# Kernel optimization log

Hardware: AMD Instinct MI355X
Metric: run time of the kernel (lower is better)

Reference implementation:

```python
import jax, jax.numpy as jnp
import numpy as np

DIM = 1024
QK = 128
HID = 2048  # int(2 * dim)
B, N = 4, 2048
EPS = 1e-5

def setup_inputs() -> dict:
    key = jax.random.key(0)
    ks = jax.random.split(key, 8)
    std = 0.02
    return {
        "x": jax.random.normal(ks[0], (B, N, DIM), jnp.float32),
        "ln_scale": jnp.ones((DIM,), jnp.float32),
        "ln_bias": jnp.zeros((DIM,), jnp.float32),
        "W_hidden": jax.random.normal(ks[1], (DIM, 2 * HID), jnp.float32) * std,
        "b_hidden": jnp.zeros((2 * HID,), jnp.float32),
        "W_qk": jax.random.normal(ks[2], (DIM, QK), jnp.float32) * std,
        "b_qk": jnp.zeros((QK,), jnp.float32),
        "os_weight": jax.random.normal(ks[3], (2, QK), jnp.float32) * std,
        "os_bias": jnp.zeros((2, QK), jnp.float32),
        "W_out": jax.random.normal(ks[4], (HID, DIM), jnp.float32) * std,
        "b_out": jnp.zeros((DIM,), jnp.float32),
    }

def reference(x, ln_scale, ln_bias, W_hidden, b_hidden, W_qk, b_qk,
              os_weight, os_bias, W_out, b_out):
    n = x.shape[1]
    # LayerNorm over last dim
    mu = jnp.mean(x, axis=-1, keepdims=True)
    var = jnp.mean(jnp.square(x - mu), axis=-1, keepdims=True)
    xn = (x - mu) / jnp.sqrt(var + EPS) * ln_scale + ln_bias
    # to_hidden: Linear + SiLU, chunk into v, gate
    hid = jax.nn.silu(xn @ W_hidden + b_hidden)          # [B,N,2*HID]
    v, gate = hid[..., :HID], hid[..., HID:]
    # to_qk: Linear + SiLU
    qk = jax.nn.silu(xn @ W_qk + b_qk)                   # [B,N,QK]
    # offset_scale: per-head elementwise affine -> q, k
    qk2 = qk[..., None, :] * os_weight + os_bias         # [B,N,2,QK]
    q, k = qk2[..., 0, :], qk2[..., 1, :]
    # ReLU^2 attention
    sim = jnp.einsum('bid,bjd->bij', q, k) / n           # [B,N,N]
    attn = jnp.square(jax.nn.relu(sim))
    out = jnp.einsum('bij,bjd->bid', attn, v)            # [B,N,HID]
    out = out * gate
    return out @ W_out + b_out
```

## Files before the change

### kernel.cpp

```cpp
#include <hip/hip_runtime.h>
#include <math.h>

#define DIMX 1024
#define QKD  128
#define HIDD 2048
#define BATCH 4
#define SEQ  2048

typedef __bf16 bf16;
typedef __bf16 bf16x8 __attribute__((ext_vector_type(8)));
typedef __bf16 bf16x4v __attribute__((ext_vector_type(4)));
typedef float f32x4 __attribute__((ext_vector_type(4)));

__device__ __forceinline__ float siluf(float v) { return v / (1.f + expf(-v)); }
__device__ __forceinline__ void splitf(float x, bf16& h, bf16& l) {
    h = (bf16)x;
    l = (bf16)(x - (float)h);
}
__device__ __forceinline__ f32x4 mfma16(bf16x8 a, bf16x8 b, f32x4 c) {
    return __builtin_amdgcn_mfma_f32_16x16x32_bf16(a, b, c, 0, 0, 0);
}

typedef __attribute__((address_space(1))) const void cg_void;
typedef __attribute__((address_space(3))) void lds_void_t;
__device__ __forceinline__ void gload16(const bf16* g, bf16* l) {
    __builtin_amdgcn_global_load_lds((cg_void*)g, (lds_void_t*)l, 16, 0, 0);
}

template<int N> __device__ __forceinline__ void wait_vm() {
    if constexpr (N == 0)  asm volatile("s_waitcnt vmcnt(0)" ::: "memory");
    if constexpr (N == 3)  asm volatile("s_waitcnt vmcnt(3)" ::: "memory");
    if constexpr (N == 4)  asm volatile("s_waitcnt vmcnt(4)" ::: "memory");
    if constexpr (N == 6)  asm volatile("s_waitcnt vmcnt(6)" ::: "memory");
    if constexpr (N == 8)  asm volatile("s_waitcnt vmcnt(8)" ::: "memory");
}

#define SB0 __builtin_amdgcn_sched_barrier(0)

__global__ __launch_bounds__(256) void ln_split(const float* __restrict__ x,
                                                const float* __restrict__ scale,
                                                const float* __restrict__ bias,
                                                bf16* __restrict__ xh,
                                                bf16* __restrict__ xl) {
    const int row = blockIdx.x;
    const float4 v = reinterpret_cast<const float4*>(x + (size_t)row * DIMX)[threadIdx.x];
    float s  = v.x + v.y + v.z + v.w;
    float ss = v.x * v.x + v.y * v.y + v.z * v.z + v.w * v.w;
    #pragma unroll
    for (int off = 32; off; off >>= 1) {
        s  += __shfl_down(s, off);
        ss += __shfl_down(ss, off);
    }
    __shared__ float ls[4], lss[4];
    const int wid = threadIdx.x >> 6, lane = threadIdx.x & 63;
    if (lane == 0) { ls[wid] = s; lss[wid] = ss; }
    __syncthreads();
    if (threadIdx.x == 0) {
        float a = ls[0] + ls[1] + ls[2] + ls[3];
        float b = lss[0] + lss[1] + lss[2] + lss[3];
        float mu  = a / DIMX;
        float var = b / DIMX - mu * mu;
        ls[0]  = mu;
        lss[0] = rsqrtf(var + 1e-5f);
    }
    __syncthreads();
    const float mu = ls[0], rs = lss[0];
    const float4 sc = reinterpret_cast<const float4*>(scale)[threadIdx.x];
    const float4 bi = reinterpret_cast<const float4*>(bias)[threadIdx.x];
    float o[4];
    o[0] = (v.x - mu) * rs * sc.x + bi.x;
    o[1] = (v.y - mu) * rs * sc.y + bi.y;
    o[2] = (v.z - mu) * rs * sc.z + bi.z;
    o[3] = (v.w - mu) * rs * sc.w + bi.w;
    bf16x4v h, l;
    #pragma unroll
    for (int i = 0; i < 4; ++i) { bf16 hh, ll; splitf(o[i], hh, ll); h[i] = hh; l[i] = ll; }
    *reinterpret_cast<bf16x4v*>(xh + (size_t)row * DIMX + threadIdx.x * 4) = h;
    *reinterpret_cast<bf16x4v*>(xl + (size_t)row * DIMX + threadIdx.x * 4) = l;
}

__global__ __launch_bounds__(256) void wsplitT(const float* __restrict__ W, int K, int N,
                                               bf16* __restrict__ Th, bf16* __restrict__ Tl) {
    __shared__ float tile[32][33];
    const int bx = blockIdx.x * 32;
    const int by = blockIdx.y * 32;
    const int tx = threadIdx.x & 31, ty = threadIdx.x >> 5;
    #pragma unroll
    for (int r = 0; r < 32; r += 8)
        tile[ty + r][tx] = W[(size_t)(by + ty + r) * N + bx + tx];
    __syncthreads();
    #pragma unroll
    for (int r = 0; r < 32; r += 8) {
        const float v = tile[tx][ty + r];
        bf16 h, l; splitf(v, h, l);
        Th[(size_t)(bx + ty + r) * K + by + tx] = h;
        if (Tl) Tl[(size_t)(bx + ty + r) * K + by + tx] = l;
    }
}

template<int EPI, int BN>
__global__ __launch_bounds__(512) void gmm2(
    const bf16* __restrict__ A, int lda, long long sA,
    const bf16* __restrict__ B, int ldb, long long sB,
    bf16* __restrict__ O, int ldo, long long sO,
    bf16* __restrict__ G, int ldg, long long sG,
    float* __restrict__ F, int ldf,
    const float* __restrict__ e0,
    int K) {

    constexpr int BM = 256, BK = 32;
    constexpr int AE = BM * BK;
    constexpr int BE = BN * BK;
    constexpr int CHA = AE / (512 * 8);
    constexpr int CHB = BE / (512 * 8);
    constexpr int L = CHA + CHB;
    constexpr int WN = BN / 4;
    constexpr int MI = 8, NI = WN / 16;

    __shared__ __align__(16) bf16 lds[4 * (AE + BE)];

    const int z = blockIdx.z;
    A += (size_t)sA * z;
    B += (size_t)sB * z;
    bf16* Oz = O ? O + (size_t)sO * z : nullptr;
    bf16* Gz = G ? G + (size_t)sG * z : nullptr;

    const int tid = threadIdx.x;
    const int l = tid & 63, w = tid >> 6;
    const int wr = w >> 2, wc = w & 3;
    const int lr = l & 15, ls4 = l >> 4;
    const int bm = blockIdx.y * BM, bn = blockIdx.x * BN;

    const bf16* aptr[CHA];
    #pragma unroll
    for (int c = 0; c < CHA; ++c) {
        const int flat = c * 512 + tid;
        const int row = flat >> 2;
        const int slot = (flat & 3) ^ ((row >> 1) & 3);
        aptr[c] = A + (size_t)(bm + row) * lda + slot * 8;
    }
    const bf16* bptr[CHB];
    #pragma unroll
    for (int c = 0; c < CHB; ++c) {
        const int flat = c * 512 + tid;
        const int row = flat >> 2;
        const int slot = (flat & 3) ^ ((row >> 1) & 3);
        bptr[c] = B + (size_t)(bn + row) * ldb + slot * 8;
    }

    int aoff[MI], boff[NI];
    #pragma unroll
    for (int i = 0; i < MI; ++i) {
        const int row = wr * 128 + i * 16 + lr;
        aoff[i] = row * BK + (ls4 ^ ((row >> 1) & 3)) * 8;
    }
    #pragma unroll
    for (int j = 0; j < NI; ++j) {
        const int row = wc * WN + j * 16 + lr;
        boff[j] = row * BK + (ls4 ^ ((row >> 1) & 3)) * 8;
    }

    const int NT = K / BK;
    f32x4 acc[MI][NI] = {};

    auto stage = [&](int tile) {
        const int buf = tile & 3;
        bf16* ab = lds + buf * (AE + BE);
        bf16* bb = ab + AE;
        #pragma unroll
        for (int c = 0; c < CHA; ++c)
            gload16(aptr[c] + tile * BK, ab + (c * 512 + w * 64) * 8);
        #pragma unroll
        for (int c = 0; c < CHB; ++c)
            gload16(bptr[c] + tile * BK, bb + (c * 512 + w * 64) * 8);
    };

    stage(0); SB0;
    stage(1); SB0;
    stage(2); SB0;

    for (int t = 0; t < NT; ++t) {
        const int ahead = NT - 1 - t;
        if (ahead >= 2)      wait_vm<2 * L>();
        else if (ahead == 1) wait_vm<L>();
        else                 wait_vm<0>();
        __builtin_amdgcn_s_barrier();
        SB0;

        const int buf = t & 3;
        const bf16* ab = lds + buf * (AE + BE);
        const bf16* bb = ab + AE;
        bf16x8 bfr[NI], afr[MI];
        #pragma unroll
        for (int j = 0; j < NI; ++j)
            bfr[j] = *reinterpret_cast<const bf16x8*>(&bb[boff[j]]);
        #pragma unroll
        for (int i = 0; i < MI; ++i)
            afr[i] = *reinterpret_cast<const bf16x8*>(&ab[aoff[i]]);
        asm volatile("s_waitcnt lgkmcnt(0)" ::: "memory");
        SB0;
        if (t + 3 < NT) { stage(t + 3); }
        SB0;
        __builtin_amdgcn_s_setprio(1);
        #pragma unroll
        for (int i = 0; i < MI; ++i)
            #pragma unroll
            for (int j = 0; j < NI; ++j)
                acc[i][j] = mfma16(afr[i], bfr[j], acc[i][j]);
        __builtin_amdgcn_s_setprio(0);
        SB0;
    }

    #pragma unroll
    for (int i = 0; i < MI; ++i) {
        const int mf = bm + wr * 128 + i * 16 + ls4 * 4;
        #pragma unroll
        for (int j = 0; j < NI; ++j) {
            const int nn = bn + wc * WN + j * 16 + lr;
            const f32x4 a = acc[i][j];
            if constexpr (EPI == 0) {
                float s[4];
                #pragma unroll
                for (int r = 0; r < 4; ++r) s[r] = siluf(a[r] + e0[nn]);
                bf16x4v h;
                #pragma unroll
                for (int r = 0; r < 4; ++r) h[r] = (bf16)s[r];
                if (nn < HIDD)
                    *reinterpret_cast<bf16x4v*>(&Oz[(size_t)nn * ldo + mf]) = h;
                else
                    *reinterpret_cast<bf16x4v*>(&Gz[(size_t)(nn - HIDD) * ldg + mf]) = h;
            } else if constexpr (EPI == 3) {
                const bf16x4v g4 = *reinterpret_cast<const bf16x4v*>(&Gz[(size_t)nn * ldg + mf]);
                #pragma unroll
                for (int r = 0; r < 4; ++r)
                    Oz[(size_t)(mf + r) * ldo + nn] = (bf16)(a[r] * (float)g4[r]);
            } else {
                #pragma unroll
                for (int r = 0; r < 4; ++r)
                    F[(size_t)(mf + r) * ldf + nn] = a[r] + e0[nn];
            }
        }
    }
}

template<int EPI, bool SPLIT, int MI, int NI>
__global__ __launch_bounds__(256) void gmm(
    const bf16* __restrict__ Ah, const bf16* __restrict__ Al, int lda, long long sA,
    const bf16* __restrict__ Bh, const bf16* __restrict__ Bl, int ldb, long long sB,
    bf16* __restrict__ O, int ldo, long long sO,
    bf16* __restrict__ O2, bf16* __restrict__ O3, bf16* __restrict__ O4,
    const float* __restrict__ e0, const float* __restrict__ e1, const float* __restrict__ e2,
    int K, float scale) {

    constexpr int TM = MI * 32, TN = NI * 32;
    constexpr int CHA = TM / 64, CHB = TN / 64;
    __shared__ __align__(16) bf16 As[TM * 32];
    __shared__ __align__(16) bf16 Bs[TN * 32];

    const int z = blockIdx.z;
    Ah += (size_t)sA * z;
    if (SPLIT) Al += (size_t)sA * z;
    Bh += (size_t)sB * z;
    if (SPLIT) Bl += (size_t)sB * z;
    if (O) O += (size_t)sO * z;

    const int t = threadIdx.x;
    const int l = t & 63, w = t >> 6;
    const int wr = w >> 1, wc = w & 1;
    const int lr = l & 15, ls = l >> 4;
    const int bm = blockIdx.y * TM, bn = blockIdx.x * TN;

    f32x4 acc[MI][NI] = {};
    const int KT = SPLIT ? 3 * K : K;

    for (int k0 = 0; k0 < KT; k0 += 32) {
        const bf16 *pA, *pB;
        int kin;
        if constexpr (SPLIT) {
            if (k0 < K)          { pA = Ah; pB = Bh; kin = k0; }
            else if (k0 < 2 * K) { pA = Al; pB = Bh; kin = k0 - K; }
            else                 { pA = Ah; pB = Bl; kin = k0 - 2 * K; }
        } else { pA = Ah; pB = Bh; kin = k0; }

        #pragma unroll
        for (int c = 0; c < CHA; ++c) {
            const int idx = c * 256 + w * 64 + l;
            const int row = idx >> 2;
            const int sg = (idx & 3) ^ ((row >> 1) & 3);
            gload16(pA + (size_t)(bm + row) * lda + kin + sg * 8,
                    As + (size_t)(c * 256 + w * 64) * 8);
        }
        #pragma unroll
        for (int c = 0; c < CHB; ++c) {
            const int idx = c * 256 + w * 64 + l;
            const int row = idx >> 2;
            const int sg = (idx & 3) ^ ((row >> 1) & 3);
            gload16(pB + (size_t)(bn + row) * ldb + kin + sg * 8,
                    Bs + (size_t)(c * 256 + w * 64) * 8);
        }
        __syncthreads();

        bf16x8 bfr[NI];
        #pragma unroll
        for (int j = 0; j < NI; ++j) {
            const int row = wc * (NI * 16) + j * 16 + lr;
            const int sl = ls ^ ((row >> 1) & 3);
            bfr[j] = *reinterpret_cast<const bf16x8*>(&Bs[row * 32 + sl * 8]);
        }
        #pragma unroll
        for (int i = 0; i < MI; ++i) {
            const int row = wr * (MI * 16) + i * 16 + lr;
            const int sl = ls ^ ((row >> 1) & 3);
            const bf16x8 af = *reinterpret_cast<const bf16x8*>(&As[row * 32 + sl * 8]);
            #pragma unroll
            for (int j = 0; j < NI; ++j)
                acc[i][j] = mfma16(af, bfr[j], acc[i][j]);
        }
        __syncthreads();
    }

    #pragma unroll
    for (int i = 0; i < MI; ++i) {
        const int mf = bm + wr * (MI * 16) + i * 16 + ls * 4;
        #pragma unroll
        for (int j = 0; j < NI; ++j) {
            const int nn = bn + wc * (NI * 16) + j * 16 + lr;
            const f32x4 a = acc[i][j];
            if constexpr (EPI == 1) {
                #pragma unroll
                for (int r = 0; r < 4; ++r) {
                    const float s = siluf(a[r] + e0[nn]);
                    const float q = s * e1[nn] + e2[nn];
                    const float k = s * e1[QKD + nn] + e2[QKD + nn];
                    bf16 h, lo;
                    splitf(q, h, lo);
                    O[(size_t)(mf + r) * ldo + nn] = h;  O2[(size_t)(mf + r) * ldo + nn] = lo;
                    splitf(k, h, lo);
                    O3[(size_t)(mf + r) * ldo + nn] = h; O4[(size_t)(mf + r) * ldo + nn] = lo;
                }
            } else if constexpr (EPI == 2) {
                #pragma unroll
                for (int r = 0; r < 4; ++r) {
                    const float tv = a[r] * scale;
                    const float p = tv > 0.f ? tv * tv : 0.f;
                    O[(size_t)(mf + r) * ldo + nn] = (bf16)p;
                }
            }
        }
    }
}

extern "C" void kernel_launch(void* const* d_in, const int* in_sizes, int n_in,
                              void* d_out, int out_size, void* d_ws, size_t ws_size,
                              hipStream_t stream) {
    const float* x        = (const float*)d_in[0];
    const float* ln_scale = (const float*)d_in[1];
    const float* ln_bias  = (const float*)d_in[2];
    const float* W_hidden = (const float*)d_in[3];
    const float* b_hidden = (const float*)d_in[4];
    const float* W_qk     = (const float*)d_in[5];
    const float* b_qk     = (const float*)d_in[6];
    const float* os_w     = (const float*)d_in[7];
    const float* os_b     = (const float*)d_in[8];
    const float* W_out    = (const float*)d_in[9];
    const float* b_out    = (const float*)d_in[10];
    float* out = (float*)d_out;

    char* p = (char*)d_ws;
    bf16* WhTh  = (bf16*)p; p += (size_t)4096 * 1024 * 2;
    bf16* WqkTh = (bf16*)p; p += (size_t)128 * 1024 * 2;
    bf16* WqkTl = (bf16*)p; p += (size_t)128 * 1024 * 2;
    bf16* WoTh  = (bf16*)p; p += (size_t)1024 * 2048 * 2;

    wsplitT<<<dim3(4096 / 32, 1024 / 32), 256, 0, stream>>>(W_hidden, 1024, 4096, WhTh, nullptr);
    wsplitT<<<dim3(128 / 32, 1024 / 32), 256, 0, stream>>>(W_qk, 1024, 128, WqkTh, WqkTl);
    wsplitT<<<dim3(1024 / 32, 2048 / 32), 256, 0, stream>>>(W_out, 2048, 1024, WoTh, nullptr);

    const size_t used = (size_t)(p - (char*)d_ws);
    const size_t qkB   = (size_t)4 * 8192 * 128 * 2;
    const size_t vTB   = (size_t)2048 * 8192 * 2;
    const size_t gateB = (size_t)2048 * 8192 * 2;
    const size_t attnB = (size_t)4 * 2048 * 2048 * 2;
    const size_t yB    = (size_t)8192 * 2048 * 2;
    const bool allb = (ws_size >= used + qkB + vTB + gateB + attnB + yB + (1u << 20));

    if (allb) {
        bf16* xh = (bf16*)out;
        bf16* xl = xh + (size_t)8192 * 1024;
        bf16* qh   = (bf16*)p; p += (size_t)8192 * 128 * 2;
        bf16* ql   = (bf16*)p; p += (size_t)8192 * 128 * 2;
        bf16* kh   = (bf16*)p; p += (size_t)8192 * 128 * 2;
        bf16* kl   = (bf16*)p; p += (size_t)8192 * 128 * 2;
        bf16* vT   = (bf16*)p; p += vTB;
        bf16* gateT= (bf16*)p; p += gateB;
        bf16* attn = (bf16*)p; p += attnB;
        bf16* y    = (bf16*)p; p += yB;

        ln_split<<<8192, 256, 0, stream>>>(x, ln_scale, ln_bias, xh, xl);

        gmm2<0, 256><<<dim3(4096 / 256, 8192 / 256), 512, 0, stream>>>(
            xh, 1024, 0, WhTh, 1024, 0,
            vT, 8192, 0, gateT, 8192, 0,
            nullptr, 0, b_hidden, 1024);

        gmm<1, true, 2, 2><<<dim3(128 / 64, 8192 / 64), 256, 0, stream>>>(
            xh, xl, 1024, 0, WqkTh, WqkTl, 1024, 0,
            qh, 128, 0, ql, kh, kl,
            b_qk, os_w, os_b, 1024, 0.f);

        gmm<2, true, 4, 4><<<dim3(16, 16, 4), 256, 0, stream>>>(
            qh, ql, 128, (long long)2048 * 128, kh, kl, 128, (long long)2048 * 128,
            attn, 2048, (long long)2048 * 2048, nullptr, nullptr, nullptr,
            nullptr, nullptr, nullptr, 128, 1.0f / SEQ);

        gmm2<3, 256><<<dim3(2048 / 256, 2048 / 256, 4), 512, 0, stream>>>(
            attn, 2048, (long long)2048 * 2048, vT, 8192, 2048,
            y, 2048, (long long)2048 * 2048, gateT, 8192, 2048,
            nullptr, 0, nullptr, 2048);

        gmm2<4, 128><<<dim3(1024 / 128, 8192 / 256), 512, 0, stream>>>(
            y, 2048, 0, WoTh, 2048, 0,
            nullptr, 0, 0, nullptr, 0, 0,
            out, 1024, b_out, 2048);
    } else {
        bf16* xh = (bf16*)p; p += (size_t)8192 * 1024 * 2;
        bf16* xl = (bf16*)p; p += (size_t)8192 * 1024 * 2;
        bf16* qh   = (bf16*)p; p += (size_t)2048 * 128 * 2;
        bf16* ql   = (bf16*)p; p += (size_t)2048 * 128 * 2;
        bf16* kh   = (bf16*)p; p += (size_t)2048 * 128 * 2;
        bf16* kl   = (bf16*)p; p += (size_t)2048 * 128 * 2;
        bf16* vT   = (bf16*)p; p += (size_t)2048 * 2048 * 2;
        bf16* gateT= (bf16*)p; p += (size_t)2048 * 2048 * 2;
        bf16* attn = (bf16*)p; p += (size_t)2048 * 2048 * 2;
        bf16* y    = (bf16*)p; p += (size_t)2048 * 2048 * 2;

        ln_split<<<8192, 256, 0, stream>>>(x, ln_scale, ln_bias, xh, xl);

        for (int b = 0; b < BATCH; ++b) {
            const bf16* xhb = xh + (size_t)b * 2048 * 1024;
            const bf16* xlb = xl + (size_t)b * 2048 * 1024;

            gmm2<0, 256><<<dim3(4096 / 256, 2048 / 256), 512, 0, stream>>>(
                xhb, 1024, 0, WhTh, 1024, 0,
                vT, 2048, 0, gateT, 2048, 0,
                nullptr, 0, b_hidden, 1024);

            gmm<1, true, 2, 2><<<dim3(128 / 64, 2048 / 64), 256, 0, stream>>>(
                xhb, xlb, 1024, 0, WqkTh, WqkTl, 1024, 0,
                qh, 128, 0, ql, kh, kl,
                b_qk, os_w, os_b, 1024, 0.f);

            gmm<2, true, 4, 4><<<dim3(16, 16, 1), 256, 0, stream>>>(
                qh, ql, 128, 0, kh, kl, 128, 0,
                attn, 2048, 0, nullptr, nullptr, nullptr,
                nullptr, nullptr, nullptr, 128, 1.0f / SEQ);

            gmm2<3, 256><<<dim3(2048 / 256, 2048 / 256, 1), 512, 0, stream>>>(
                attn, 2048, 0, vT, 2048, 0,
                y, 2048, 0, gateT, 2048, 0,
                nullptr, 0, nullptr, 2048);

            gmm2<4, 128><<<dim3(1024 / 128, 2048 / 256), 512, 0, stream>>>(
                y, 2048, 0, WoTh, 2048, 0,
                nullptr, 0, 0, nullptr, 0, 0,
                out + (size_t)b * 2048 * 1024, 1024, b_out, 2048);
        }
    }
}
```

Measured before the change: 293.7 us.

## Switch big GEMMs to 128x256 tiles, triple buffering, and XCD-aware block remap

Replaces the templated gmm2 kernel with gmm5, which uses a fixed 128x256 block tile (4x4 MFMA fragments per wave) and a 3-stage LDS ring instead of a 4-stage one. It also remaps linear block IDs so that consecutive blocks on the same XCD (assuming round-robin dispatch over 8 dies) cover neighbouring tiles, which should improve L2 reuse. Smaller tiles give more blocks and less LDS per block, so occupancy and tail behaviour should improve. The cost is lower arithmetic intensity per block and a shallower prefetch depth. The remap assumes the block count is divisible by 8.

```diff
diff --git a/kernel.cpp b/kernel.cpp
--- a/kernel.cpp
+++ b/kernel.cpp
@@ -30,9 +30,7 @@
 template<int N> __device__ __forceinline__ void wait_vm() {
     if constexpr (N == 0)  asm volatile("s_waitcnt vmcnt(0)" ::: "memory");
     if constexpr (N == 3)  asm volatile("s_waitcnt vmcnt(3)" ::: "memory");
-    if constexpr (N == 4)  asm volatile("s_waitcnt vmcnt(4)" ::: "memory");
     if constexpr (N == 6)  asm volatile("s_waitcnt vmcnt(6)" ::: "memory");
-    if constexpr (N == 8)  asm volatile("s_waitcnt vmcnt(8)" ::: "memory");
 }
 
 #define SB0 __builtin_amdgcn_sched_barrier(0)
@@ -98,8 +96,8 @@
     }
 }
 
-template<int EPI, int BN>
-__global__ __launch_bounds__(512) void gmm2(
+template<int EPI>
+__global__ __launch_bounds__(512) void gmm5(
     const bf16* __restrict__ A, int lda, long long sA,
     const bf16* __restrict__ B, int ldb, long long sB,
     bf16* __restrict__ O, int ldo, long long sO,
@@ -108,16 +106,21 @@
     const float* __restrict__ e0,
     int K) {
 
-    constexpr int BM = 256, BK = 32;
+    constexpr int BM = 128, BN = 256, BK = 32;
     constexpr int AE = BM * BK;
     constexpr int BE = BN * BK;
-    constexpr int CHA = AE / (512 * 8);
-    constexpr int CHB = BE / (512 * 8);
-    constexpr int L = CHA + CHB;
-    constexpr int WN = BN / 4;
-    constexpr int MI = 8, NI = WN / 16;
-
-    __shared__ __align__(16) bf16 lds[4 * (AE + BE)];
+    constexpr int TE = AE + BE;
+    constexpr int L = 3;
+    constexpr int MI = 4, NI = 4;
+
+    __shared__ __align__(16) bf16 lds[3 * TE];
+
+    const int gx = gridDim.x;
+    const int nwg = gx * gridDim.y;
+    const int lin = blockIdx.x + gx * blockIdx.y;
+    const int qq = nwg >> 3;
+    const int nl = (lin & 7) * qq + (lin >> 3);
+    const int bm = (nl / gx) * BM, bn = (nl % gx) * BN;
 
     const int z = blockIdx.z;
     A += (size_t)sA * z;
@@ -129,19 +132,13 @@
     const int l = tid & 63, w = tid >> 6;
     const int wr = w >> 2, wc = w & 3;
     const int lr = l & 15, ls4 = l >> 4;
-    const int bm = blockIdx.y * BM, bn = blockIdx.x * BN;
-
-    const bf16* aptr[CHA];
-    #pragma unroll
-    for (int c = 0; c < CHA; ++c) {
-        const int flat = c * 512 + tid;
-        const int row = flat >> 2;
-        const int slot = (flat & 3) ^ ((row >> 1) & 3);
-        aptr[c] = A + (size_t)(bm + row) * lda + slot * 8;
-    }
-    const bf16* bptr[CHB];
-    #pragma unroll
-    for (int c = 0; c < CHB; ++c) {
+
+    const int ar = tid >> 2;
+    const int as = (tid & 3) ^ ((ar >> 1) & 3);
+    const bf16* aptr = A + (size_t)(bm + ar) * lda + as * 8;
+    const bf16* bptr[2];
+    #pragma unroll
+    for (int c = 0; c < 2; ++c) {
         const int flat = c * 512 + tid;
         const int row = flat >> 2;
         const int slot = (flat & 3) ^ ((row >> 1) & 3);
@@ -151,12 +148,12 @@
     int aoff[MI], boff[NI];
     #pragma unroll
     for (int i = 0; i < MI; ++i) {
-        const int row = wr * 128 + i * 16 + lr;
+        const int row = wr * 64 + i * 16 + lr;
         aoff[i] = row * BK + (ls4 ^ ((row >> 1) & 3)) * 8;
     }
     #pragma unroll
     for (int j = 0; j < NI; ++j) {
-        const int row = wc * WN + j * 16 + lr;
+        const int row = wc * 64 + j * 16 + lr;
         boff[j] = row * BK + (ls4 ^ ((row >> 1) & 3)) * 8;
     }
 
@@ -164,42 +161,34 @@
     f32x4 acc[MI][NI] = {};
 
     auto stage = [&](int tile) {
-        const int buf = tile & 3;
-        bf16* ab = lds + buf * (AE + BE);
-        bf16* bb = ab + AE;
-        #pragma unroll
-        for (int c = 0; c < CHA; ++c)
-            gload16(aptr[c] + tile * BK, ab + (c * 512 + w * 64) * 8);
-        #pragma unroll
-        for (int c = 0; c < CHB; ++c)
-            gload16(bptr[c] + tile * BK, bb + (c * 512 + w * 64) * 8);
+        bf16* tb = lds + (tile % 3) * TE;
+        gload16(aptr + (size_t)tile * BK, tb + w * 512);
+        bf16* bb = tb + AE;
+        gload16(bptr[0] + (size_t)tile * BK, bb + w * 512);
+        gload16(bptr[1] + (size_t)tile * BK, bb + 4096 + w * 512);
     };
 
     stage(0); SB0;
     stage(1); SB0;
-    stage(2); SB0;
 
     for (int t = 0; t < NT; ++t) {
-        const int ahead = NT - 1 - t;
-        if (ahead >= 2)      wait_vm<2 * L>();
-        else if (ahead == 1) wait_vm<L>();
-        else                 wait_vm<0>();
+        if (t + 1 < NT) wait_vm<L>();
+        else            wait_vm<0>();
         __builtin_amdgcn_s_barrier();
         SB0;
 
-        const int buf = t & 3;
-        const bf16* ab = lds + buf * (AE + BE);
-        const bf16* bb = ab + AE;
-        bf16x8 bfr[NI], afr[MI];
+        const bf16* tb = lds + (t % 3) * TE;
+        const bf16* bb = tb + AE;
+        bf16x8 afr[MI], bfr[NI];
         #pragma unroll
         for (int j = 0; j < NI; ++j)
             bfr[j] = *reinterpret_cast<const bf16x8*>(&bb[boff[j]]);
         #pragma unroll
         for (int i = 0; i < MI; ++i)
-            afr[i] = *reinterpret_cast<const bf16x8*>(&ab[aoff[i]]);
+            afr[i] = *reinterpret_cast<const bf16x8*>(&tb[aoff[i]]);
         asm volatile("s_waitcnt lgkmcnt(0)" ::: "memory");
         SB0;
-        if (t + 3 < NT) { stage(t + 3); }
+        if (t + 2 < NT) { stage(t + 2); }
         SB0;
         __builtin_amdgcn_s_setprio(1);
         #pragma unroll
@@ -213,10 +202,10 @@
 
     #pragma unroll
     for (int i = 0; i < MI; ++i) {
-        const int mf = bm + wr * 128 + i * 16 + ls4 * 4;
+        const int mf = bm + wr * 64 + i * 16 + ls4 * 4;
         #pragma unroll
         for (int j = 0; j < NI; ++j) {
-            const int nn = bn + wc * WN + j * 16 + lr;
+            const int nn = bn + wc * 64 + j * 16 + lr;
             const f32x4 a = acc[i][j];
             if constexpr (EPI == 0) {
                 float s[4];
@@ -398,7 +387,7 @@
 
         ln_split<<<8192, 256, 0, stream>>>(x, ln_scale, ln_bias, xh, xl);
 
-        gmm2<0, 256><<<dim3(4096 / 256, 8192 / 256), 512, 0, stream>>>(
+        gmm5<0><<<dim3(4096 / 256, 8192 / 128), 512, 0, stream>>>(
             xh, 1024, 0, WhTh, 1024, 0,
             vT, 8192, 0, gateT, 8192, 0,
             nullptr, 0, b_hidden, 1024);
@@ -413,12 +402,12 @@
             attn, 2048, (long long)2048 * 2048, nullptr, nullptr, nullptr,
             nullptr, nullptr, nullptr, 128, 1.0f / SEQ);
 
-        gmm2<3, 256><<<dim3(2048 / 256, 2048 / 256, 4), 512, 0, stream>>>(
+        gmm5<3><<<dim3(2048 / 256, 2048 / 128, 4), 512, 0, stream>>>(
             attn, 2048, (long long)2048 * 2048, vT, 8192, 2048,
             y, 2048, (long long)2048 * 2048, gateT, 8192, 2048,
             nullptr, 0, nullptr, 2048);
 
-        gmm2<4, 128><<<dim3(1024 / 128, 8192 / 256), 512, 0, stream>>>(
+        gmm5<4><<<dim3(1024 / 256, 8192 / 128), 512, 0, stream>>>(
             y, 2048, 0, WoTh, 2048, 0,
             nullptr, 0, 0, nullptr, 0, 0,
             out, 1024, b_out, 2048);
@@ -440,7 +429,7 @@
             const bf16* xhb = xh + (size_t)b * 2048 * 1024;
             const bf16* xlb = xl + (size_t)b * 2048 * 1024;
 
-            gmm2<0, 256><<<dim3(4096 / 256, 2048 / 256), 512, 0, stream>>>(
+            gmm5<0><<<dim3(4096 / 256, 2048 / 128), 512, 0, stream>>>(
                 xhb, 1024, 0, WhTh, 1024, 0,
                 vT, 2048, 0, gateT, 2048, 0,
                 nullptr, 0, b_hidden, 1024);
@@ -455,12 +444,12 @@
                 attn, 2048, 0, nullptr, nullptr, nullptr,
                 nullptr, nullptr, nullptr, 128, 1.0f / SEQ);
 
-            gmm2<3, 256><<<dim3(2048 / 256, 2048 / 256, 1), 512, 0, stream>>>(
+            gmm5<3><<<dim3(2048 / 256, 2048 / 128, 1), 512, 0, stream>>>(
                 attn, 2048, 0, vT, 2048, 0,
                 y, 2048, 0, gateT, 2048, 0,
                 nullptr, 0, nullptr, 2048);
 
-            gmm2<4, 128><<<dim3(1024 / 128, 2048 / 256), 512, 0, stream>>>(
+            gmm5<4><<<dim3(1024 / 256, 2048 / 128), 512, 0, stream>>>(
                 y, 2048, 0, WoTh, 2048, 0,
                 nullptr, 0, 0, nullptr, 0, 0,
                 out + (size_t)b * 2048 * 1024, 1024, b_out, 2048);
```

Result: no change. 298.5 us (+1.6%).

## Replace 4-stage BK=32 GEMM pipeline with double-buffered BK=64 and XCD-aware block remap

Applied to the files above, without the earlier changes.

The main bf16 GEMM kernel changes from a 4-deep ring of 32-wide K tiles with fine-grained vmcnt waits to a 2-buffer scheme that loads 64-wide K steps, separated by one __syncthreads per step. It also remaps the linear workgroup id so that consecutive blocks spread across the 8 dies, for better L2 locality, and makes the output GEMM use a 128x256 tile instead of 256x128. The aim is fewer barriers per K and better cache behaviour. The cost is less prefetch depth and a full barrier where the old code waited only on outstanding loads, and the setprio hints are removed.

```diff
diff --git a/kernel.cpp b/kernel.cpp
--- a/kernel.cpp
+++ b/kernel.cpp
@@ -25,14 +25,6 @@
 typedef __attribute__((address_space(3))) void lds_void_t;
 __device__ __forceinline__ void gload16(const bf16* g, bf16* l) {
     __builtin_amdgcn_global_load_lds((cg_void*)g, (lds_void_t*)l, 16, 0, 0);
-}
-
-template<int N> __device__ __forceinline__ void wait_vm() {
-    if constexpr (N == 0)  asm volatile("s_waitcnt vmcnt(0)" ::: "memory");
-    if constexpr (N == 3)  asm volatile("s_waitcnt vmcnt(3)" ::: "memory");
-    if constexpr (N == 4)  asm volatile("s_waitcnt vmcnt(4)" ::: "memory");
-    if constexpr (N == 6)  asm volatile("s_waitcnt vmcnt(6)" ::: "memory");
-    if constexpr (N == 8)  asm volatile("s_waitcnt vmcnt(8)" ::: "memory");
 }
 
 #define SB0 __builtin_amdgcn_sched_barrier(0)
@@ -98,8 +90,8 @@
     }
 }
 
-template<int EPI, int BN>
-__global__ __launch_bounds__(512) void gmm2(
+template<int EPI, int BM>
+__global__ __launch_bounds__(512) void gmm7(
     const bf16* __restrict__ A, int lda, long long sA,
     const bf16* __restrict__ B, int ldb, long long sB,
     bf16* __restrict__ O, int ldo, long long sO,
@@ -108,16 +100,23 @@
     const float* __restrict__ e0,
     int K) {
 
-    constexpr int BM = 256, BK = 32;
-    constexpr int AE = BM * BK;
-    constexpr int BE = BN * BK;
+    constexpr int BN = 256;
+    constexpr int AE = BM * 32;
+    constexpr int BE = BN * 32;
+    constexpr int PE = AE + BE;
+    constexpr int HALF = 2 * PE;
     constexpr int CHA = AE / (512 * 8);
     constexpr int CHB = BE / (512 * 8);
-    constexpr int L = CHA + CHB;
-    constexpr int WN = BN / 4;
-    constexpr int MI = 8, NI = WN / 16;
-
-    __shared__ __align__(16) bf16 lds[4 * (AE + BE)];
+    constexpr int MI = BM / 32, NI = 4;
+
+    __shared__ __align__(16) bf16 lds[2 * HALF];
+
+    const int gx = gridDim.x;
+    const int nwg = gx * gridDim.y;
+    const int lin = blockIdx.x + gx * blockIdx.y;
+    const int qq = nwg >> 3;
+    const int nl = (lin & 7) * qq + (lin >> 3);
+    const int bm = (nl / gx) * BM, bn = (nl % gx) * BN;
 
     const int z = blockIdx.z;
     A += (size_t)sA * z;
@@ -129,7 +128,6 @@
     const int l = tid & 63, w = tid >> 6;
     const int wr = w >> 2, wc = w & 3;
     const int lr = l & 15, ls4 = l >> 4;
-    const int bm = blockIdx.y * BM, bn = blockIdx.x * BN;
 
     const bf16* aptr[CHA];
     #pragma unroll
@@ -151,72 +149,65 @@
     int aoff[MI], boff[NI];
     #pragma unroll
     for (int i = 0; i < MI; ++i) {
-        const int row = wr * 128 + i * 16 + lr;
-        aoff[i] = row * BK + (ls4 ^ ((row >> 1) & 3)) * 8;
+        const int row = wr * (BM / 2) + i * 16 + lr;
+        aoff[i] = row * 32 + (ls4 ^ ((row >> 1) & 3)) * 8;
     }
     #pragma unroll
     for (int j = 0; j < NI; ++j) {
-        const int row = wc * WN + j * 16 + lr;
-        boff[j] = row * BK + (ls4 ^ ((row >> 1) & 3)) * 8;
-    }
-
-    const int NT = K / BK;
+        const int row = wc * 64 + j * 16 + lr;
+        boff[j] = row * 32 + (ls4 ^ ((row >> 1) & 3)) * 8;
+    }
+
+    const int NT = K / 64;
     f32x4 acc[MI][NI] = {};
 
-    auto stage = [&](int tile) {
-        const int buf = tile & 3;
-        bf16* ab = lds + buf * (AE + BE);
-        bf16* bb = ab + AE;
-        #pragma unroll
-        for (int c = 0; c < CHA; ++c)
-            gload16(aptr[c] + tile * BK, ab + (c * 512 + w * 64) * 8);
-        #pragma unroll
-        for (int c = 0; c < CHB; ++c)
-            gload16(bptr[c] + tile * BK, bb + (c * 512 + w * 64) * 8);
+    auto stage64 = [&](int t) {
+        bf16* bb = lds + (t & 1) * HALF;
+        #pragma unroll
+        for (int h = 0; h < 2; ++h) {
+            bf16* pb = bb + h * PE;
+            const size_t ko = (size_t)t * 64 + h * 32;
+            #pragma unroll
+            for (int c = 0; c < CHA; ++c)
+                gload16(aptr[c] + ko, pb + (c * 512 + w * 64) * 8);
+            #pragma unroll
+            for (int c = 0; c < CHB; ++c)
+                gload16(bptr[c] + ko, pb + AE + (c * 512 + w * 64) * 8);
+        }
     };
 
-    stage(0); SB0;
-    stage(1); SB0;
-    stage(2); SB0;
+    stage64(0);
 
     for (int t = 0; t < NT; ++t) {
-        const int ahead = NT - 1 - t;
-        if (ahead >= 2)      wait_vm<2 * L>();
-        else if (ahead == 1) wait_vm<L>();
-        else                 wait_vm<0>();
-        __builtin_amdgcn_s_barrier();
+        __syncthreads();
+        if (t + 1 < NT) stage64(t + 1);
         SB0;
 
-        const int buf = t & 3;
-        const bf16* ab = lds + buf * (AE + BE);
-        const bf16* bb = ab + AE;
-        bf16x8 bfr[NI], afr[MI];
-        #pragma unroll
-        for (int j = 0; j < NI; ++j)
-            bfr[j] = *reinterpret_cast<const bf16x8*>(&bb[boff[j]]);
-        #pragma unroll
-        for (int i = 0; i < MI; ++i)
-            afr[i] = *reinterpret_cast<const bf16x8*>(&ab[aoff[i]]);
-        asm volatile("s_waitcnt lgkmcnt(0)" ::: "memory");
-        SB0;
-        if (t + 3 < NT) { stage(t + 3); }
-        SB0;
-        __builtin_amdgcn_s_setprio(1);
-        #pragma unroll
-        for (int i = 0; i < MI; ++i)
+        const bf16* bb = lds + (t & 1) * HALF;
+        #pragma unroll
+        for (int h = 0; h < 2; ++h) {
+            const bf16* pb = bb + h * PE;
+            bf16x8 afr[MI], bfr[NI];
             #pragma unroll
             for (int j = 0; j < NI; ++j)
-                acc[i][j] = mfma16(afr[i], bfr[j], acc[i][j]);
-        __builtin_amdgcn_s_setprio(0);
-        SB0;
+                bfr[j] = *reinterpret_cast<const bf16x8*>(&pb[AE + boff[j]]);
+            #pragma unroll
+            for (int i = 0; i < MI; ++i)
+                afr[i] = *reinterpret_cast<const bf16x8*>(&pb[aoff[i]]);
+            #pragma unroll
+            for (int i = 0; i < MI; ++i)
+                #pragma unroll
+                for (int j = 0; j < NI; ++j)
+                    acc[i][j] = mfma16(afr[i], bfr[j], acc[i][j]);
+        }
     }
 
     #pragma unroll
     for (int i = 0; i < MI; ++i) {
-        const int mf = bm + wr * 128 + i * 16 + ls4 * 4;
+        const int mf = bm + wr * (BM / 2) + i * 16 + ls4 * 4;
         #pragma unroll
         for (int j = 0; j < NI; ++j) {
-            const int nn = bn + wc * WN + j * 16 + lr;
+            const int nn = bn + wc * 64 + j * 16 + lr;
             const f32x4 a = acc[i][j];
             if constexpr (EPI == 0) {
                 float s[4];
@@ -398,7 +389,7 @@
 
         ln_split<<<8192, 256, 0, stream>>>(x, ln_scale, ln_bias, xh, xl);
 
-        gmm2<0, 256><<<dim3(4096 / 256, 8192 / 256), 512, 0, stream>>>(
+        gmm7<0, 256><<<dim3(4096 / 256, 8192 / 256), 512, 0, stream>>>(
             xh, 1024, 0, WhTh, 1024, 0,
             vT, 8192, 0, gateT, 8192, 0,
             nullptr, 0, b_hidden, 1024);
@@ -413,12 +404,12 @@
             attn, 2048, (long long)2048 * 2048, nullptr, nullptr, nullptr,
             nullptr, nullptr, nullptr, 128, 1.0f / SEQ);
 
-        gmm2<3, 256><<<dim3(2048 / 256, 2048 / 256, 4), 512, 0, stream>>>(
+        gmm7<3, 256><<<dim3(2048 / 256, 2048 / 256, 4), 512, 0, stream>>>(
             attn, 2048, (long long)2048 * 2048, vT, 8192, 2048,
             y, 2048, (long long)2048 * 2048, gateT, 8192, 2048,
             nullptr, 0, nullptr, 2048);
 
-        gmm2<4, 128><<<dim3(1024 / 128, 8192 / 256), 512, 0, stream>>>(
+        gmm7<4, 128><<<dim3(1024 / 256, 8192 / 128), 512, 0, stream>>>(
             y, 2048, 0, WoTh, 2048, 0,
             nullptr, 0, 0, nullptr, 0, 0,
             out, 1024, b_out, 2048);
@@ -440,7 +431,7 @@
             const bf16* xhb = xh + (size_t)b * 2048 * 1024;
             const bf16* xlb = xl + (size_t)b * 2048 * 1024;
 
-            gmm2<0, 256><<<dim3(4096 / 256, 2048 / 256), 512, 0, stream>>>(
+            gmm7<0, 256><<<dim3(4096 / 256, 2048 / 256), 512, 0, stream>>>(
                 xhb, 1024, 0, WhTh, 1024, 0,
                 vT, 2048, 0, gateT, 2048, 0,
                 nullptr, 0, b_hidden, 1024);
@@ -455,12 +446,12 @@
                 attn, 2048, 0, nullptr, nullptr, nullptr,
                 nullptr, nullptr, nullptr, 128, 1.0f / SEQ);
 
-            gmm2<3, 256><<<dim3(2048 / 256, 2048 / 256, 1), 512, 0, stream>>>(
+            gmm7<3, 256><<<dim3(2048 / 256, 2048 / 256, 1), 512, 0, stream>>>(
                 attn, 2048, 0, vT, 2048, 0,
                 y, 2048, 0, gateT, 2048, 0,
                 nullptr, 0, nullptr, 2048);
 
-            gmm2<4, 128><<<dim3(1024 / 128, 2048 / 256), 512, 0, stream>>>(
+            gmm7<4, 128><<<dim3(1024 / 256, 2048 / 128), 512, 0, stream>>>(
                 y, 2048, 0, WoTh, 2048, 0,
                 nullptr, 0, 0, nullptr, 0, 0,
                 out + (size_t)b * 2048 * 1024, 1024, b_out, 2048);
```

Result: no change. 294.0 us (+0.1%).

## Split hidden projection into swapped-operand V GEMM and row-major gate GEMM

Applied to the files above, without the earlier changes.

The single fused hidden GEMM, whose epilogue wrote both v and gate transposed with 4-element strided stores, becomes two launches. The v half runs with operands swapped, so its output tile is produced directly in the transposed layout and stored along contiguous rows. The gate half is stored row-major, so the attention·V epilogue reads the gate with the same indexing as its output. This aims to remove strided scattered stores and gate reads, at the cost of an extra launch and scalar per-element stores.

```diff
diff --git a/kernel.cpp b/kernel.cpp
--- a/kernel.cpp
+++ b/kernel.cpp
@@ -218,22 +218,24 @@
         for (int j = 0; j < NI; ++j) {
             const int nn = bn + wc * WN + j * 16 + lr;
             const f32x4 a = acc[i][j];
-            if constexpr (EPI == 0) {
-                float s[4];
-                #pragma unroll
-                for (int r = 0; r < 4; ++r) s[r] = siluf(a[r] + e0[nn]);
-                bf16x4v h;
-                #pragma unroll
-                for (int r = 0; r < 4; ++r) h[r] = (bf16)s[r];
-                if (nn < HIDD)
-                    *reinterpret_cast<bf16x4v*>(&Oz[(size_t)nn * ldo + mf]) = h;
-                else
-                    *reinterpret_cast<bf16x4v*>(&Gz[(size_t)(nn - HIDD) * ldg + mf]) = h;
+            if constexpr (EPI == 5) {
+                #pragma unroll
+                for (int r = 0; r < 4; ++r) {
+                    const float s = siluf(a[r] + e0[mf + r]);
+                    Oz[(size_t)(mf + r) * ldo + nn] = (bf16)s;
+                }
+            } else if constexpr (EPI == 6) {
+                #pragma unroll
+                for (int r = 0; r < 4; ++r) {
+                    const float s = siluf(a[r] + e0[nn]);
+                    Oz[(size_t)(mf + r) * ldo + nn] = (bf16)s;
+                }
             } else if constexpr (EPI == 3) {
-                const bf16x4v g4 = *reinterpret_cast<const bf16x4v*>(&Gz[(size_t)nn * ldg + mf]);
-                #pragma unroll
-                for (int r = 0; r < 4; ++r)
-                    Oz[(size_t)(mf + r) * ldo + nn] = (bf16)(a[r] * (float)g4[r]);
+                #pragma unroll
+                for (int r = 0; r < 4; ++r) {
+                    const float g = (float)Gz[(size_t)(mf + r) * ldg + nn];
+                    Oz[(size_t)(mf + r) * ldo + nn] = (bf16)(a[r] * g);
+                }
             } else {
                 #pragma unroll
                 for (int r = 0; r < 4; ++r)
@@ -379,7 +381,7 @@
     const size_t used = (size_t)(p - (char*)d_ws);
     const size_t qkB   = (size_t)4 * 8192 * 128 * 2;
     const size_t vTB   = (size_t)2048 * 8192 * 2;
-    const size_t gateB = (size_t)2048 * 8192 * 2;
+    const size_t gateB = (size_t)8192 * 2048 * 2;
     const size_t attnB = (size_t)4 * 2048 * 2048 * 2;
     const size_t yB    = (size_t)8192 * 2048 * 2;
     const bool allb = (ws_size >= used + qkB + vTB + gateB + attnB + yB + (1u << 20));
@@ -392,16 +394,21 @@
         bf16* kh   = (bf16*)p; p += (size_t)8192 * 128 * 2;
         bf16* kl   = (bf16*)p; p += (size_t)8192 * 128 * 2;
         bf16* vT   = (bf16*)p; p += vTB;
-        bf16* gateT= (bf16*)p; p += gateB;
+        bf16* gate = (bf16*)p; p += gateB;
         bf16* attn = (bf16*)p; p += attnB;
         bf16* y    = (bf16*)p; p += yB;
 
         ln_split<<<8192, 256, 0, stream>>>(x, ln_scale, ln_bias, xh, xl);
 
-        gmm2<0, 256><<<dim3(4096 / 256, 8192 / 256), 512, 0, stream>>>(
-            xh, 1024, 0, WhTh, 1024, 0,
-            vT, 8192, 0, gateT, 8192, 0,
+        gmm2<5, 256><<<dim3(8192 / 256, 2048 / 256), 512, 0, stream>>>(
+            WhTh, 1024, 0, xh, 1024, 0,
+            vT, 8192, 0, nullptr, 0, 0,
             nullptr, 0, b_hidden, 1024);
+
+        gmm2<6, 256><<<dim3(2048 / 256, 8192 / 256), 512, 0, stream>>>(
+            xh, 1024, 0, WhTh + (size_t)2048 * 1024, 1024, 0,
+            gate, 2048, 0, nullptr, 0, 0,
+            nullptr, 0, b_hidden + HIDD, 1024);
 
         gmm<1, true, 2, 2><<<dim3(128 / 64, 8192 / 64), 256, 0, stream>>>(
             xh, xl, 1024, 0, WqkTh, WqkTl, 1024, 0,
@@ -415,7 +422,7 @@
 
         gmm2<3, 256><<<dim3(2048 / 256, 2048 / 256, 4), 512, 0, stream>>>(
             attn, 2048, (long long)2048 * 2048, vT, 8192, 2048,
-            y, 2048, (long long)2048 * 2048, gateT, 8192, 2048,
+            y, 2048, (long long)2048 * 2048, gate, 2048, (long long)2048 * 2048,
             nullptr, 0, nullptr, 2048);
 
         gmm2<4, 128><<<dim3(1024 / 128, 8192 / 256), 512, 0, stream>>>(
@@ -430,7 +437,7 @@
         bf16* kh   = (bf16*)p; p += (size_t)2048 * 128 * 2;
         bf16* kl   = (bf16*)p; p += (size_t)2048 * 128 * 2;
         bf16* vT   = (bf16*)p; p += (size_t)2048 * 2048 * 2;
-        bf16* gateT= (bf16*)p; p += (size_t)2048 * 2048 * 2;
+        bf16* gate = (bf16*)p; p += (size_t)2048 * 2048 * 2;
         bf16* attn = (bf16*)p; p += (size_t)2048 * 2048 * 2;
         bf16* y    = (bf16*)p; p += (size_t)2048 * 2048 * 2;
 
@@ -440,10 +447,15 @@
             const bf16* xhb = xh + (size_t)b * 2048 * 1024;
             const bf16* xlb = xl + (size_t)b * 2048 * 1024;
 
-            gmm2<0, 256><<<dim3(4096 / 256, 2048 / 256), 512, 0, stream>>>(
-                xhb, 1024, 0, WhTh, 1024, 0,
-                vT, 2048, 0, gateT, 2048, 0,
+            gmm2<5, 256><<<dim3(2048 / 256, 2048 / 256), 512, 0, stream>>>(
+                WhTh, 1024, 0, xhb, 1024, 0,
+                vT, 2048, 0, nullptr, 0, 0,
                 nullptr, 0, b_hidden, 1024);
+
+            gmm2<6, 256><<<dim3(2048 / 256, 2048 / 256), 512, 0, stream>>>(
+                xhb, 1024, 0, WhTh + (size_t)2048 * 1024, 1024, 0,
+                gate, 2048, 0, nullptr, 0, 0,
+                nullptr, 0, b_hidden + HIDD, 1024);
 
             gmm<1, true, 2, 2><<<dim3(128 / 64, 2048 / 64), 256, 0, stream>>>(
                 xhb, xlb, 1024, 0, WqkTh, WqkTl, 1024, 0,
@@ -457,7 +469,7 @@
 
             gmm2<3, 256><<<dim3(2048 / 256, 2048 / 256, 1), 512, 0, stream>>>(
                 attn, 2048, 0, vT, 2048, 0,
-                y, 2048, 0, gateT, 2048, 0,
+                y, 2048, 0, gate, 2048, 0,
                 nullptr, 0, nullptr, 2048);
 
             gmm2<4, 128><<<dim3(1024 / 128, 2048 / 256), 512, 0, stream>>>(
```

Measured after the change: 293.5 us. About the same (-0.1%).
